# Performance work log

Measured on AMD Instinct MI355X. Metric: run time of the kernel, lower is better.

The kernel has to match this reference:

```python
import jax, jax.numpy as jnp
import numpy as np
from jax import lax

# Dimensions (ModelArgs with d_model=1024)
B, L = 2, 1024
D_MODEL = 1024
D_INNER = 2048          # expand * d_model
D_STATE = 16
DT_RANK = 64            # ceil(d_model / 16)
D_CONV = 4


def setup_inputs() -> dict:
    key = jax.random.key(0)
    ks = jax.random.split(key, 8)
    sc = lambda k, shp, s: jax.random.normal(k, shp, dtype=jnp.float32) * s
    x = jax.random.normal(ks[0], (B, L, D_MODEL), dtype=jnp.float32)
    W_in = sc(ks[1], (2 * D_INNER, D_MODEL), 0.02)
    conv_w = sc(ks[2], (D_INNER, D_CONV), 0.2)
    conv_b = jnp.zeros((D_INNER,), jnp.float32)
    W_x = sc(ks[3], (DT_RANK + 2 * D_STATE, D_INNER), 0.02)
    dt_init_std = DT_RANK ** -0.5
    W_dt = jax.random.uniform(ks[4], (D_INNER, DT_RANK), jnp.float32,
                              -dt_init_std, dt_init_std)
    # dt_proj bias: inverse-softplus of dt ~ logUniform(dt_min, dt_max)
    dt_min, dt_max = 1e-3, 1e-1
    u = jax.random.uniform(ks[5], (D_INNER,), jnp.float32)
    dt = jnp.exp(u * (np.log(dt_max) - np.log(dt_min)) + np.log(dt_min))
    dt = jnp.clip(dt, 1e-4, None)
    b_dt = dt + jnp.log(-jnp.expm1(-dt))
    A_log = jnp.log(jnp.tile(jnp.arange(1, D_STATE + 1, dtype=jnp.float32)[None, :],
                             (D_INNER, 1)))
    D = jnp.ones((D_INNER,), jnp.float32)
    W_out = sc(ks[6], (D_MODEL, D_INNER), 0.02)
    return {"x": x, "W_in": W_in, "conv_w": conv_w, "conv_b": conv_b,
            "W_x": W_x, "W_dt": W_dt, "b_dt": b_dt, "A_log": A_log,
            "D": D, "W_out": W_out}


def reference(x, W_in, conv_w, conv_b, W_x, W_dt, b_dt, A_log, D, W_out):
    b, l, _ = x.shape
    d_in, n = A_log.shape
    k = conv_w.shape[1]

    # in_proj, split into conv branch and gating residual
    x_and_res = x @ W_in.T                                 # (b, l, 2*d_in)
    xz, res = jnp.split(x_and_res, [d_in], axis=-1)

    # Causal depthwise conv1d (kernel k, left-pad k-1, truncate to l)
    xp = jnp.pad(xz, ((0, 0), (k - 1, 0), (0, 0)))         # (b, l+k-1, d_in)
    xc = conv_b[None, None, :] + sum(
        xp[:, i:i + l, :] * conv_w[None, None, :, i] for i in range(k))
    xc = jax.nn.silu(xc)                                   # (b, l, d_in)

    # x_proj -> delta, B, C
    x_dbl = xc @ W_x.T                                     # (b, l, dt_rank+2n)
    dlt, Bm, Cm = jnp.split(x_dbl, [DT_RANK, DT_RANK + n], axis=-1)
    delta = jax.nn.softplus(dlt @ W_dt.T + b_dt)           # (b, l, d_in)

    # selective scan
    A = -jnp.exp(A_log)                                    # (d_in, n)
    dA = jnp.exp(delta[..., None] * A[None, None])         # (b, l, d_in, n)
    dBu = (delta * xc)[..., None] * Bm[:, :, None, :]      # (b, l, d_in, n)

    def step(h, inp):
        dA_t, dBu_t, C_t = inp                             # (b,d,n),(b,d,n),(b,n)
        h = dA_t * h + dBu_t
        y = jnp.einsum('bdn,bn->bd', h, C_t)
        return h, y

    h0 = jnp.zeros((b, d_in, n), xc.dtype)
    _, ys = lax.scan(step, h0, (dA.transpose(1, 0, 2, 3),
                                dBu.transpose(1, 0, 2, 3),
                                Cm.transpose(1, 0, 2)))
    y = ys.transpose(1, 0, 2) + xc * D[None, None, :]      # (b, l, d_in)

    y = y * jax.nn.silu(res)
    return y @ W_out.T                                     # (b, l, d_model)
```

## Files before the change

### kernel.cpp

```cpp
#include <hip/hip_runtime.h>
#include <hip/hip_bf16.h>
#include <cmath>

#define DEV __device__ __forceinline__

typedef float  f32x4  __attribute__((ext_vector_type(4)));
typedef __bf16 bf16x8 __attribute__((ext_vector_type(8)));
using u16 = unsigned short;

constexpr int CB   = 2;
constexpr int CLEN = 1024;
constexpr int CDM  = 1024;
constexpr int CDI  = 2048;
constexpr int CM   = CB * CLEN;
constexpr int NCHUNK = 32;
constexpr int CHL    = 32;

DEV u16 f2bf(float f) {
  unsigned u = __builtin_bit_cast(unsigned, f);
  unsigned r = (u + 0x7fffu + ((u >> 16) & 1u)) >> 16;
  return (u16)r;
}
DEV float bf2f(u16 v) { return __builtin_bit_cast(float, ((unsigned)v) << 16); }

DEV ushort4 f4bf(float4 v) {
  ushort4 o;
  o.x = f2bf(v.x); o.y = f2bf(v.y); o.z = f2bf(v.z); o.w = f2bf(v.w);
  return o;
}

constexpr int CG_X   = 524288;
constexpr int CG_WIN = CG_X   + 1048576;
constexpr int CG_WDT = CG_WIN + 32768;
constexpr int CG_WO  = CG_WDT + 524288;
constexpr int CG_WX  = CG_WO  + 65536;

__global__ void cast_all_k(const float* __restrict__ x, const float* __restrict__ W_in,
                           const float* __restrict__ W_dt, const float* __restrict__ W_out,
                           const float* __restrict__ W_x,
                           u16* __restrict__ xb, u16* __restrict__ W_inb,
                           u16* __restrict__ W_dtb, u16* __restrict__ W_outb,
                           u16* __restrict__ W_xb)
{
  int i = blockIdx.x * blockDim.x + threadIdx.x;
  if (i < CG_X) {
    reinterpret_cast<ushort4*>(xb)[i] = f4bf(reinterpret_cast<const float4*>(x)[i]);
  } else if (i < CG_WIN) {
    int j = i - CG_X;
    reinterpret_cast<ushort4*>(W_inb)[j] = f4bf(reinterpret_cast<const float4*>(W_in)[j]);
  } else if (i < CG_WDT) {
    int j = i - CG_WIN;
    reinterpret_cast<ushort4*>(W_dtb)[j] = f4bf(reinterpret_cast<const float4*>(W_dt)[j]);
  } else if (i < CG_WO) {
    int j = i - CG_WDT;
    reinterpret_cast<ushort4*>(W_outb)[j] = f4bf(reinterpret_cast<const float4*>(W_out)[j]);
  } else {
    int j = i - CG_WO;
    int base = j * 4, row = base >> 11, col = base & 2047;
    float4 v = make_float4(0.f, 0.f, 0.f, 0.f);
    if (row < 96) v = *reinterpret_cast<const float4*>(W_x + row * 2048 + col);
    reinterpret_cast<ushort4*>(W_xb)[j] = f4bf(v);
  }
}

template <int EPI, int SPLITK>
__global__ __launch_bounds__(256, 2)
void gemm_bt(const u16* __restrict__ A, const u16* __restrict__ Bw,
             float* __restrict__ C, u16* __restrict__ Cb,
             const float* __restrict__ bias,
             int Nd, int Kd, int lda, int ldb, int ldc, size_t slice_stride)
{
  __shared__ u16 As[128 * 32];
  __shared__ u16 Bs[128 * 32];
  const int tid  = threadIdx.x;
  const int wave = tid >> 6;
  const int lane = tid & 63;
  const int wm = wave >> 1, wn = wave & 1;
  const int row0 = blockIdx.y * 128;
  const int col0 = blockIdx.x * 128;
  const int lr = lane >> 2;
  const int lc = (lane & 3) * 8;

  const int kper = Kd / SPLITK;
  const int kbeg = (SPLITK > 1) ? blockIdx.z * kper : 0;
  const int kend = kbeg + kper;
  float* Cz = (SPLITK > 1) ? C + (size_t)blockIdx.z * slice_stride : C;

  const u16* Ag = A  + (size_t)(row0 + wave * 16 + lr) * lda + lc;
  const u16* Bg = Bw + (size_t)(col0 + wave * 16 + lr) * ldb + lc;
  u16* Al0 = As + (wave * 16 + lr) * 32 + lc;
  u16* Al1 = As + (64 + wave * 16 + lr) * 32 + lc;
  u16* Bl0 = Bs + (wave * 16 + lr) * 32 + lc;
  u16* Bl1 = Bs + (64 + wave * 16 + lr) * 32 + lc;

  bf16x8 pa0 = *reinterpret_cast<const bf16x8*>(Ag + kbeg);
  bf16x8 pa1 = *reinterpret_cast<const bf16x8*>(Ag + (size_t)64 * lda + kbeg);
  bf16x8 pb0 = *reinterpret_cast<const bf16x8*>(Bg + kbeg);
  bf16x8 pb1 = *reinterpret_cast<const bf16x8*>(Bg + (size_t)64 * ldb + kbeg);

  f32x4 acc[4][4] = {};
  const int q  = lane >> 4;
  const int mr = lane & 15;

  for (int k0 = kbeg; k0 < kend; k0 += 32) {
    __syncthreads();
    *reinterpret_cast<bf16x8*>(Al0) = pa0;
    *reinterpret_cast<bf16x8*>(Al1) = pa1;
    *reinterpret_cast<bf16x8*>(Bl0) = pb0;
    *reinterpret_cast<bf16x8*>(Bl1) = pb1;
    __syncthreads();
    const int k1 = (k0 + 32 < kend) ? k0 + 32 : kbeg;
    pa0 = *reinterpret_cast<const bf16x8*>(Ag + k1);
    pa1 = *reinterpret_cast<const bf16x8*>(Ag + (size_t)64 * lda + k1);
    pb0 = *reinterpret_cast<const bf16x8*>(Bg + k1);
    pb1 = *reinterpret_cast<const bf16x8*>(Bg + (size_t)64 * ldb + k1);

    bf16x8 af[4], bfr[4];
#pragma unroll
    for (int t = 0; t < 4; ++t) {
      af[t]  = *reinterpret_cast<const bf16x8*>(As + (wm * 64 + t * 16 + mr) * 32 + q * 8);
      bfr[t] = *reinterpret_cast<const bf16x8*>(Bs + (wn * 64 + t * 16 + mr) * 32 + q * 8);
    }
#pragma unroll
    for (int mt = 0; mt < 4; ++mt)
#pragma unroll
      for (int nt = 0; nt < 4; ++nt)
        acc[mt][nt] = __builtin_amdgcn_mfma_f32_16x16x32_bf16(af[mt], bfr[nt], acc[mt][nt], 0, 0, 0);
  }

  const int cn = lane & 15;
#pragma unroll
  for (int mt = 0; mt < 4; ++mt)
#pragma unroll
    for (int nt = 0; nt < 4; ++nt)
#pragma unroll
      for (int r = 0; r < 4; ++r) {
        const int row = row0 + wm * 64 + mt * 16 + q * 4 + r;
        const int col = col0 + wn * 64 + nt * 16 + cn;
        float v = acc[mt][nt][r];
        if (EPI == 3) {
          v += bias[col];
          v = (v > 15.f) ? v : log1pf(__expf(v));
        }
        if (EPI == 0) Cz[(size_t)row * ldc + col] = v;
        else          Cb[(size_t)row * ldc + col] = f2bf(v);
      }
}

__global__ void xdbl_reduce_k(const float* __restrict__ part,
                              float* __restrict__ xdbl, u16* __restrict__ xdblb)
{
  int i = blockIdx.x * blockDim.x + threadIdx.x;
  float4 s = reinterpret_cast<const float4*>(part)[i];
#pragma unroll
  for (int z = 1; z < 16; ++z) {
    float4 p = reinterpret_cast<const float4*>(part + (size_t)z * CM * 128)[i];
    s.x += p.x; s.y += p.y; s.z += p.z; s.w += p.w;
  }
  reinterpret_cast<float4*>(xdbl)[i] = s;
  reinterpret_cast<ushort4*>(xdblb)[i] = f4bf(s);
}

__global__ void out_reduce_k(const float* __restrict__ part, float* __restrict__ out)
{
  int i = blockIdx.x * blockDim.x + threadIdx.x;
  float4 s = reinterpret_cast<const float4*>(part)[i];
#pragma unroll
  for (int z = 1; z < 4; ++z) {
    float4 p = reinterpret_cast<const float4*>(part + (size_t)z * CM * CDM)[i];
    s.x += p.x; s.y += p.y; s.z += p.z; s.w += p.w;
  }
  reinterpret_cast<float4*>(out)[i] = s;
}

__global__ void conv_silu_k(const u16* __restrict__ xzb, const float4* __restrict__ cw4,
                            const float* __restrict__ cb, u16* __restrict__ xcb)
{
  int idx = blockIdx.x * blockDim.x + threadIdx.x;
  int d   = idx & (CDI - 1);
  int row = idx >> 11;
  int l   = row & (CLEN - 1);
  float4 wv = cw4[d];
  const float* wp = (const float*)&wv;
  float acc = cb[d];
#pragma unroll
  for (int i = 0; i < 4; ++i) {
    int ls = l - 3 + i;
    float v = (ls >= 0) ? bf2f(xzb[(size_t)(row - l + ls) * 4096 + d]) : 0.f;
    acc += v * wp[i];
  }
  float s = acc / (1.f + __expf(-acc));
  xcb[idx] = f2bf(s);
}

__global__ __launch_bounds__(256)
void scan_p1(const u16* __restrict__ delta_b, const u16* __restrict__ xcb,
             const float* __restrict__ xdbl, const float* __restrict__ A_log,
             float* __restrict__ P, float* __restrict__ S)
{
  __shared__ float sB[CHL * 16];
  const int t = threadIdx.x;
  const int d = blockIdx.x * 256 + t;
  const int c = blockIdx.y, b = blockIdx.z;

  for (int i = t; i < CHL * 16; i += 256) {
    int ll = i >> 4, n = i & 15;
    sB[i] = xdbl[(size_t)(b * CLEN + c * CHL + ll) * 128 + 64 + n];
  }
  __syncthreads();

  float An[16], Pv[16], Sv[16];
#pragma unroll
  for (int n = 0; n < 16; ++n) {
    An[n] = -__expf(A_log[d * 16 + n]);
    Pv[n] = 1.f; Sv[n] = 0.f;
  }
  const size_t rbase = (size_t)(b * CLEN + c * CHL) * CDI + d;
  for (int ll = 0; ll < CHL; ++ll) {
    float dl = bf2f(delta_b[rbase + (size_t)ll * CDI]);
    float u  = bf2f(xcb[rbase + (size_t)ll * CDI]);
    float du = dl * u;
#pragma unroll
    for (int n = 0; n < 16; ++n) {
      float a = __expf(dl * An[n]);
      Pv[n] *= a;
      Sv[n] = a * Sv[n] + du * sB[ll * 16 + n];
    }
  }
  const size_t o = (size_t)((b * NCHUNK + c) * 16) * CDI + d;
#pragma unroll
  for (int n = 0; n < 16; ++n) {
    P[o + (size_t)n * CDI] = Pv[n];
    S[o + (size_t)n * CDI] = Sv[n];
  }
}

__global__ void scan_p2(const float* __restrict__ P, const float* __restrict__ S,
                        float* __restrict__ Hin)
{
  const int t = threadIdx.x;
  const int d = blockIdx.x * 256 + t;
  const int n = blockIdx.y, b = blockIdx.z;
  float h = 0.f;
#pragma unroll 8
  for (int c = 0; c < NCHUNK; ++c) {
    size_t o = (size_t)((b * NCHUNK + c) * 16 + n) * CDI + d;
    Hin[o] = h;
    h = P[o] * h + S[o];
  }
}

__global__ __launch_bounds__(256)
void scan_p3(const u16* __restrict__ delta_b, const u16* __restrict__ xcb,
             const float* __restrict__ xdbl, const float* __restrict__ A_log,
             const float* __restrict__ Dvec, const u16* __restrict__ xzb,
             const float* __restrict__ Hin, u16* __restrict__ ybarb)
{
  __shared__ float sB[CHL * 16];
  __shared__ float sC[CHL * 16];
  const int t = threadIdx.x;
  const int d = blockIdx.x * 256 + t;
  const int c = blockIdx.y, b = blockIdx.z;

  for (int i = t; i < CHL * 16; i += 256) {
    int ll = i >> 4, n = i & 15;
    size_t ro = (size_t)(b * CLEN + c * CHL + ll) * 128;
    sB[i] = xdbl[ro + 64 + n];
    sC[i] = xdbl[ro + 80 + n];
  }
  __syncthreads();

  float An[16], h[16];
  const size_t ho = (size_t)((b * NCHUNK + c) * 16) * CDI + d;
#pragma unroll
  for (int n = 0; n < 16; ++n) {
    An[n] = -__expf(A_log[d * 16 + n]);
    h[n]  = Hin[ho + (size_t)n * CDI];
  }
  const float Dd = Dvec[d];
  const size_t rbase = (size_t)(b * CLEN + c * CHL);
  for (int ll = 0; ll < CHL; ++ll) {
    size_t e = (rbase + ll) * CDI + d;
    float dl = bf2f(delta_b[e]);
    float u  = bf2f(xcb[e]);
    float du = dl * u;
    float y  = 0.f;
#pragma unroll
    for (int n = 0; n < 16; ++n) {
      float a = __expf(dl * An[n]);
      h[n] = a * h[n] + du * sB[ll * 16 + n];
      y += h[n] * sC[ll * 16 + n];
    }
    y += u * Dd;
    float r = bf2f(xzb[(rbase + ll) * 4096 + CDI + d]);
    float sr = r / (1.f + __expf(-r));
    ybarb[e] = f2bf(y * sr);
  }
}

extern "C" void kernel_launch(void* const* d_in, const int* in_sizes, int n_in,
                              void* d_out, int out_size, void* d_ws, size_t ws_size,
                              hipStream_t stream)
{
  (void)in_sizes; (void)n_in; (void)out_size; (void)ws_size;
  const float* x      = (const float*)d_in[0];
  const float* W_in   = (const float*)d_in[1];
  const float* conv_w = (const float*)d_in[2];
  const float* conv_b = (const float*)d_in[3];
  const float* W_x    = (const float*)d_in[4];
  const float* W_dt   = (const float*)d_in[5];
  const float* b_dt   = (const float*)d_in[6];
  const float* A_log  = (const float*)d_in[7];
  const float* Dvec   = (const float*)d_in[8];
  const float* W_out  = (const float*)d_in[9];
  float* out = (float*)d_out;

  constexpr size_t MB = 1048576;
  char* w = (char*)d_ws;
  u16*   xzres_b = (u16*)(w + 0);
  u16*   xb      = (u16*)(w + 16 * MB);
  u16*   W_inb   = (u16*)(w + 20 * MB);
  u16*   xcb     = (u16*)(w + 28 * MB);
  u16*   delta_b = (u16*)(w + 36 * MB);
  float* xpart   = (float*)(w + 44 * MB);
  float* xdbl    = (float*)(w + 60 * MB);
  u16*   xdblb   = (u16*)(w + 61 * MB);
  u16*   W_xb    = (u16*)(w + 61 * MB + 512 * 1024);
  u16*   W_dtb   = (u16*)(w + 62 * MB);
  float* Pb      = (float*)(w + 63 * MB);
  float* Sb      = (float*)(w + 71 * MB);
  float* Hin     = (float*)(w + 79 * MB);
  u16*   ybarb   = (u16*)(w + 87 * MB);
  u16*   W_outb  = (u16*)(w + 95 * MB);
  float* opart   = (float*)(w + 99 * MB);

  dim3 blk(256);
  cast_all_k<<<CG_WX / 256, blk, 0, stream>>>(x, W_in, W_dt, W_out, W_x,
                                              xb, W_inb, W_dtb, W_outb, W_xb);
  gemm_bt<1, 1><<<dim3(32, 16), blk, 0, stream>>>(xb, W_inb, nullptr, xzres_b, nullptr,
                                                  4096, 1024, 1024, 1024, 4096, 0);
  conv_silu_k<<<(CB * CLEN * CDI) / 256, blk, 0, stream>>>(xzres_b, (const float4*)conv_w,
                                                           conv_b, xcb);
  gemm_bt<0, 16><<<dim3(1, 16, 16), blk, 0, stream>>>(xcb, W_xb, xpart, nullptr, nullptr,
                                                      128, 2048, 2048, 2048, 128,
                                                      (size_t)CM * 128);
  xdbl_reduce_k<<<(CM * 128 / 4) / 256, blk, 0, stream>>>(xpart, xdbl, xdblb);
  gemm_bt<3, 1><<<dim3(16, 16), blk, 0, stream>>>(xdblb, W_dtb, nullptr, delta_b, b_dt,
                                                  2048, 64, 128, 64, 2048, 0);
  scan_p1<<<dim3(8, NCHUNK, 2), blk, 0, stream>>>(delta_b, xcb, xdbl, A_log, Pb, Sb);
  scan_p2<<<dim3(8, 16, 2), blk, 0, stream>>>(Pb, Sb, Hin);
  scan_p3<<<dim3(8, NCHUNK, 2), blk, 0, stream>>>(delta_b, xcb, xdbl, A_log, Dvec,
                                                  xzres_b, Hin, ybarb);
  gemm_bt<0, 4><<<dim3(8, 16, 4), blk, 0, stream>>>(ybarb, W_outb, opart, nullptr, nullptr,
                                                    1024, 2048, 2048, 2048, 1024,
                                                    (size_t)CM * CDM);
  out_reduce_k<<<(CM * CDM / 4) / 256, blk, 0, stream>>>(opart, out);
}
```

Before: 250.6 us.

## Fuse fp32-to-bf16 casts into GEMM tile loads and vectorize conv

Removes the separate cast kernel by letting the GEMM template read fp32 operands directly and convert them to bf16 while staging into shared memory. The x_proj weight, which has 96 rows, is now zero-padded in registers instead of through a padded bf16 copy. The depthwise conv+SiLU kernel now handles 8 channels per thread with 16-byte vector loads and stores. This saves one launch and a full read/write pass over the weights and input. In exchange, every GEMM now reads fp32 weights (twice the bytes) and re-converts them for each tile, including repeatedly across row blocks.

```diff
diff --git a/kernel.cpp b/kernel.cpp
--- a/kernel.cpp
+++ b/kernel.cpp
@@ -23,53 +23,22 @@
 }
 DEV float bf2f(u16 v) { return __builtin_bit_cast(float, ((unsigned)v) << 16); }
 
-DEV ushort4 f4bf(float4 v) {
-  ushort4 o;
-  o.x = f2bf(v.x); o.y = f2bf(v.y); o.z = f2bf(v.z); o.w = f2bf(v.w);
-  return o;
-}
-
-constexpr int CG_X   = 524288;
-constexpr int CG_WIN = CG_X   + 1048576;
-constexpr int CG_WDT = CG_WIN + 32768;
-constexpr int CG_WO  = CG_WDT + 524288;
-constexpr int CG_WX  = CG_WO  + 65536;
-
-__global__ void cast_all_k(const float* __restrict__ x, const float* __restrict__ W_in,
-                           const float* __restrict__ W_dt, const float* __restrict__ W_out,
-                           const float* __restrict__ W_x,
-                           u16* __restrict__ xb, u16* __restrict__ W_inb,
-                           u16* __restrict__ W_dtb, u16* __restrict__ W_outb,
-                           u16* __restrict__ W_xb)
-{
-  int i = blockIdx.x * blockDim.x + threadIdx.x;
-  if (i < CG_X) {
-    reinterpret_cast<ushort4*>(xb)[i] = f4bf(reinterpret_cast<const float4*>(x)[i]);
-  } else if (i < CG_WIN) {
-    int j = i - CG_X;
-    reinterpret_cast<ushort4*>(W_inb)[j] = f4bf(reinterpret_cast<const float4*>(W_in)[j]);
-  } else if (i < CG_WDT) {
-    int j = i - CG_WIN;
-    reinterpret_cast<ushort4*>(W_dtb)[j] = f4bf(reinterpret_cast<const float4*>(W_dt)[j]);
-  } else if (i < CG_WO) {
-    int j = i - CG_WDT;
-    reinterpret_cast<ushort4*>(W_outb)[j] = f4bf(reinterpret_cast<const float4*>(W_out)[j]);
-  } else {
-    int j = i - CG_WO;
-    int base = j * 4, row = base >> 11, col = base & 2047;
-    float4 v = make_float4(0.f, 0.f, 0.f, 0.f);
-    if (row < 96) v = *reinterpret_cast<const float4*>(W_x + row * 2048 + col);
-    reinterpret_cast<ushort4*>(W_xb)[j] = f4bf(v);
-  }
-}
-
-template <int EPI, int SPLITK>
+DEV bf16x8 cvt8(float4 a, float4 b) {
+  bf16x8 r;
+  r[0] = (__bf16)a.x; r[1] = (__bf16)a.y; r[2] = (__bf16)a.z; r[3] = (__bf16)a.w;
+  r[4] = (__bf16)b.x; r[5] = (__bf16)b.y; r[6] = (__bf16)b.z; r[7] = (__bf16)b.w;
+  return r;
+}
+
+template <int EPI, int SPLITK, bool AF32, bool BF32, bool PADB>
 __global__ __launch_bounds__(256, 2)
-void gemm_bt(const u16* __restrict__ A, const u16* __restrict__ Bw,
+void gemm_bt(const void* __restrict__ Av, const void* __restrict__ Bv,
              float* __restrict__ C, u16* __restrict__ Cb,
              const float* __restrict__ bias,
              int Nd, int Kd, int lda, int ldb, int ldc, size_t slice_stride)
 {
+  constexpr size_t ASZ = AF32 ? 4 : 2;
+  constexpr size_t BSZ = BF32 ? 4 : 2;
   __shared__ u16 As[128 * 32];
   __shared__ u16 Bs[128 * 32];
   const int tid  = threadIdx.x;
@@ -86,17 +55,55 @@
   const int kend = kbeg + kper;
   float* Cz = (SPLITK > 1) ? C + (size_t)blockIdx.z * slice_stride : C;
 
-  const u16* Ag = A  + (size_t)(row0 + wave * 16 + lr) * lda + lc;
-  const u16* Bg = Bw + (size_t)(col0 + wave * 16 + lr) * ldb + lc;
+  const char* Ag = (const char*)Av + ((size_t)(row0 + wave * 16 + lr) * lda + lc) * ASZ;
+  const char* Bg = (const char*)Bv + ((size_t)(col0 + wave * 16 + lr) * ldb + lc) * BSZ;
+  const size_t Astep64 = (size_t)64 * lda * ASZ;
+  const size_t Bstep64 = (size_t)64 * ldb * BSZ;
+  const bool b1ok = !PADB || (col0 + 64 + wave * 16 + lr) < 96;
+
   u16* Al0 = As + (wave * 16 + lr) * 32 + lc;
   u16* Al1 = As + (64 + wave * 16 + lr) * 32 + lc;
   u16* Bl0 = Bs + (wave * 16 + lr) * 32 + lc;
   u16* Bl1 = Bs + (64 + wave * 16 + lr) * 32 + lc;
 
-  bf16x8 pa0 = *reinterpret_cast<const bf16x8*>(Ag + kbeg);
-  bf16x8 pa1 = *reinterpret_cast<const bf16x8*>(Ag + (size_t)64 * lda + kbeg);
-  bf16x8 pb0 = *reinterpret_cast<const bf16x8*>(Bg + kbeg);
-  bf16x8 pb1 = *reinterpret_cast<const bf16x8*>(Bg + (size_t)64 * ldb + kbeg);
+  float4 paf[2][2], pbf[2][2];
+  bf16x8 pah[2], pbh[2];
+
+  auto ld_tile = [&](int k) {
+    if constexpr (AF32) {
+      paf[0][0] = *(const float4*)(Ag + (size_t)k * 4);
+      paf[0][1] = *(const float4*)(Ag + (size_t)k * 4 + 16);
+      paf[1][0] = *(const float4*)(Ag + Astep64 + (size_t)k * 4);
+      paf[1][1] = *(const float4*)(Ag + Astep64 + (size_t)k * 4 + 16);
+    } else {
+      pah[0] = *(const bf16x8*)(Ag + (size_t)k * 2);
+      pah[1] = *(const bf16x8*)(Ag + Astep64 + (size_t)k * 2);
+    }
+    if constexpr (BF32) {
+      pbf[0][0] = *(const float4*)(Bg + (size_t)k * 4);
+      pbf[0][1] = *(const float4*)(Bg + (size_t)k * 4 + 16);
+      if (b1ok) {
+        pbf[1][0] = *(const float4*)(Bg + Bstep64 + (size_t)k * 4);
+        pbf[1][1] = *(const float4*)(Bg + Bstep64 + (size_t)k * 4 + 16);
+      }
+    } else {
+      pbh[0] = *(const bf16x8*)(Bg + (size_t)k * 2);
+      if (b1ok) pbh[1] = *(const bf16x8*)(Bg + Bstep64 + (size_t)k * 2);
+    }
+  };
+
+  auto st_tile = [&]() {
+    bf16x8 a0, a1, b0, b1;
+    if constexpr (AF32) { a0 = cvt8(paf[0][0], paf[0][1]); a1 = cvt8(paf[1][0], paf[1][1]); }
+    else                { a0 = pah[0]; a1 = pah[1]; }
+    if constexpr (BF32) { b0 = cvt8(pbf[0][0], pbf[0][1]); b1 = cvt8(pbf[1][0], pbf[1][1]); }
+    else                { b0 = pbh[0]; b1 = pbh[1]; }
+    if (PADB && !b1ok) { bf16x8 z = {}; b1 = z; }
+    *(bf16x8*)Al0 = a0; *(bf16x8*)Al1 = a1;
+    *(bf16x8*)Bl0 = b0; *(bf16x8*)Bl1 = b1;
+  };
+
+  ld_tile(kbeg);
 
   f32x4 acc[4][4] = {};
   const int q  = lane >> 4;
@@ -104,16 +111,10 @@
 
   for (int k0 = kbeg; k0 < kend; k0 += 32) {
     __syncthreads();
-    *reinterpret_cast<bf16x8*>(Al0) = pa0;
-    *reinterpret_cast<bf16x8*>(Al1) = pa1;
-    *reinterpret_cast<bf16x8*>(Bl0) = pb0;
-    *reinterpret_cast<bf16x8*>(Bl1) = pb1;
+    st_tile();
     __syncthreads();
     const int k1 = (k0 + 32 < kend) ? k0 + 32 : kbeg;
-    pa0 = *reinterpret_cast<const bf16x8*>(Ag + k1);
-    pa1 = *reinterpret_cast<const bf16x8*>(Ag + (size_t)64 * lda + k1);
-    pb0 = *reinterpret_cast<const bf16x8*>(Bg + k1);
-    pb1 = *reinterpret_cast<const bf16x8*>(Bg + (size_t)64 * ldb + k1);
+    ld_tile(k1);
 
     bf16x8 af[4], bfr[4];
 #pragma unroll
@@ -158,7 +159,9 @@
     s.x += p.x; s.y += p.y; s.z += p.z; s.w += p.w;
   }
   reinterpret_cast<float4*>(xdbl)[i] = s;
-  reinterpret_cast<ushort4*>(xdblb)[i] = f4bf(s);
+  ushort4 o;
+  o.x = f2bf(s.x); o.y = f2bf(s.y); o.z = f2bf(s.z); o.w = f2bf(s.w);
+  reinterpret_cast<ushort4*>(xdblb)[i] = o;
 }
 
 __global__ void out_reduce_k(const float* __restrict__ part, float* __restrict__ out)
@@ -177,20 +180,37 @@
                             const float* __restrict__ cb, u16* __restrict__ xcb)
 {
   int idx = blockIdx.x * blockDim.x + threadIdx.x;
-  int d   = idx & (CDI - 1);
-  int row = idx >> 11;
+  int d8  = (idx & (CDI / 8 - 1)) * 8;
+  int row = idx >> 8;
   int l   = row & (CLEN - 1);
-  float4 wv = cw4[d];
-  const float* wp = (const float*)&wv;
-  float acc = cb[d];
+
+  float4 wv[8];
+#pragma unroll
+  for (int j = 0; j < 8; ++j) wv[j] = cw4[d8 + j];
+  float acc[8];
+#pragma unroll
+  for (int j = 0; j < 8; ++j) acc[j] = cb[d8 + j];
+
 #pragma unroll
   for (int i = 0; i < 4; ++i) {
     int ls = l - 3 + i;
-    float v = (ls >= 0) ? bf2f(xzb[(size_t)(row - l + ls) * 4096 + d]) : 0.f;
-    acc += v * wp[i];
-  }
-  float s = acc / (1.f + __expf(-acc));
-  xcb[idx] = f2bf(s);
+    if (ls >= 0) {
+      bf16x8 v = *reinterpret_cast<const bf16x8*>(xzb + (size_t)(row - l + ls) * 4096 + d8);
+      const float* wp;
+#pragma unroll
+      for (int j = 0; j < 8; ++j) {
+        wp = (const float*)&wv[j];
+        acc[j] += (float)v[j] * wp[i];
+      }
+    }
+  }
+  bf16x8 o;
+#pragma unroll
+  for (int j = 0; j < 8; ++j) {
+    float s = acc[j] / (1.f + __expf(-acc[j]));
+    o[j] = (__bf16)s;
+  }
+  *reinterpret_cast<bf16x8*>(xcb + (size_t)row * CDI + d8) = o;
 }
 
 __global__ __launch_bounds__(256)
@@ -318,41 +338,34 @@
   constexpr size_t MB = 1048576;
   char* w = (char*)d_ws;
   u16*   xzres_b = (u16*)(w + 0);
-  u16*   xb      = (u16*)(w + 16 * MB);
-  u16*   W_inb   = (u16*)(w + 20 * MB);
-  u16*   xcb     = (u16*)(w + 28 * MB);
-  u16*   delta_b = (u16*)(w + 36 * MB);
-  float* xpart   = (float*)(w + 44 * MB);
-  float* xdbl    = (float*)(w + 60 * MB);
-  u16*   xdblb   = (u16*)(w + 61 * MB);
-  u16*   W_xb    = (u16*)(w + 61 * MB + 512 * 1024);
-  u16*   W_dtb   = (u16*)(w + 62 * MB);
-  float* Pb      = (float*)(w + 63 * MB);
-  float* Sb      = (float*)(w + 71 * MB);
-  float* Hin     = (float*)(w + 79 * MB);
-  u16*   ybarb   = (u16*)(w + 87 * MB);
-  u16*   W_outb  = (u16*)(w + 95 * MB);
-  float* opart   = (float*)(w + 99 * MB);
+  u16*   xcb     = (u16*)(w + 16 * MB);
+  u16*   delta_b = (u16*)(w + 24 * MB);
+  float* xpart   = (float*)(w + 32 * MB);
+  float* xdbl    = (float*)(w + 48 * MB);
+  u16*   xdblb   = (u16*)(w + 49 * MB);
+  float* Pb      = (float*)(w + 50 * MB);
+  float* Sb      = (float*)(w + 58 * MB);
+  float* Hin     = (float*)(w + 66 * MB);
+  u16*   ybarb   = (u16*)(w + 74 * MB);
+  float* opart   = (float*)(w + 82 * MB);
 
   dim3 blk(256);
-  cast_all_k<<<CG_WX / 256, blk, 0, stream>>>(x, W_in, W_dt, W_out, W_x,
-                                              xb, W_inb, W_dtb, W_outb, W_xb);
-  gemm_bt<1, 1><<<dim3(32, 16), blk, 0, stream>>>(xb, W_inb, nullptr, xzres_b, nullptr,
-                                                  4096, 1024, 1024, 1024, 4096, 0);
-  conv_silu_k<<<(CB * CLEN * CDI) / 256, blk, 0, stream>>>(xzres_b, (const float4*)conv_w,
-                                                           conv_b, xcb);
-  gemm_bt<0, 16><<<dim3(1, 16, 16), blk, 0, stream>>>(xcb, W_xb, xpart, nullptr, nullptr,
-                                                      128, 2048, 2048, 2048, 128,
-                                                      (size_t)CM * 128);
+  gemm_bt<1, 1, true, true, false><<<dim3(32, 16), blk, 0, stream>>>(
+      x, W_in, nullptr, xzres_b, nullptr, 4096, 1024, 1024, 1024, 4096, 0);
+  conv_silu_k<<<(CB * CLEN * CDI / 8) / 256, blk, 0, stream>>>(
+      xzres_b, (const float4*)conv_w, conv_b, xcb);
+  gemm_bt<0, 16, false, true, true><<<dim3(1, 16, 16), blk, 0, stream>>>(
+      xcb, W_x, xpart, nullptr, nullptr, 128, 2048, 2048, 2048, 128,
+      (size_t)CM * 128);
   xdbl_reduce_k<<<(CM * 128 / 4) / 256, blk, 0, stream>>>(xpart, xdbl, xdblb);
-  gemm_bt<3, 1><<<dim3(16, 16), blk, 0, stream>>>(xdblb, W_dtb, nullptr, delta_b, b_dt,
-                                                  2048, 64, 128, 64, 2048, 0);
+  gemm_bt<3, 1, false, true, false><<<dim3(16, 16), blk, 0, stream>>>(
+      xdblb, W_dt, nullptr, delta_b, b_dt, 2048, 64, 128, 64, 2048, 0);
   scan_p1<<<dim3(8, NCHUNK, 2), blk, 0, stream>>>(delta_b, xcb, xdbl, A_log, Pb, Sb);
   scan_p2<<<dim3(8, 16, 2), blk, 0, stream>>>(Pb, Sb, Hin);
   scan_p3<<<dim3(8, NCHUNK, 2), blk, 0, stream>>>(delta_b, xcb, xdbl, A_log, Dvec,
                                                   xzres_b, Hin, ybarb);
-  gemm_bt<0, 4><<<dim3(8, 16, 4), blk, 0, stream>>>(ybarb, W_outb, opart, nullptr, nullptr,
-                                                    1024, 2048, 2048, 2048, 1024,
-                                                    (size_t)CM * CDM);
+  gemm_bt<0, 4, false, true, false><<<dim3(8, 16, 4), blk, 0, stream>>>(
+      ybarb, W_out, opart, nullptr, nullptr, 1024, 2048, 2048, 2048, 1024,
+      (size_t)CM * CDM);
   out_reduce_k<<<(CM * CDM / 4) / 256, blk, 0, stream>>>(opart, out);
 }
```

After: 266.5 us. 1.06x slower.
